# Kernel optimization log

Measured on AMD Instinct MI355X. Metric: run time of the kernel, lower is better.

Reference implementation:

```python
import jax, jax.numpy as jnp
import numpy as np

N_USERS = 50000
N_ENTITIES = 100000
N_RELATIONS = 16
N_KG_EDGES = 2000000
N_UI_EDGES = 1000000
EMB = 64
N_HEADS = 2
D_K = EMB // N_HEADS
N_HOPS = 2


def setup_inputs() -> dict:
    key = jax.random.key(0)
    ks = jax.random.split(key, 8)
    user_emb = jax.random.normal(ks[0], (N_USERS, EMB), dtype=jnp.float32)
    entity_emb = jax.random.normal(ks[1], (N_ENTITIES, EMB), dtype=jnp.float32)
    edge_index = jax.random.randint(ks[2], (2, N_KG_EDGES), 0, N_ENTITIES, dtype=jnp.int64)
    # edge_type values in [1, n_relations] because the module indexes relation_emb[edge_type - 1]
    edge_type = jax.random.randint(ks[3], (N_KG_EDGES,), 1, N_RELATIONS + 1, dtype=jnp.int64)
    inter_user = jax.random.randint(ks[4], (N_UI_EDGES,), 0, N_USERS, dtype=jnp.int64)
    inter_item = jax.random.randint(ks[5], (N_UI_EDGES,), 0, N_ENTITIES, dtype=jnp.int64)
    inter_edge = jnp.stack([inter_user, inter_item], axis=0)
    inter_edge_w = jax.random.uniform(ks[6], (N_UI_EDGES,), dtype=jnp.float32)
    # learned params (xavier-uniform W_Q, normal relation embedding)
    limit = np.sqrt(6.0 / (EMB + EMB)).astype(np.float32)
    W_Q = jax.random.uniform(ks[7], (EMB, EMB), minval=-limit, maxval=limit, dtype=jnp.float32)
    relation_emb = jax.random.normal(jax.random.fold_in(key, 99), (N_RELATIONS, EMB), dtype=jnp.float32)
    return {
        "user_emb": user_emb,
        "entity_emb": entity_emb,
        "edge_index": edge_index,
        "edge_type": edge_type,
        "inter_edge": inter_edge,
        "inter_edge_w": inter_edge_w,
        "W_Q": W_Q,
        "relation_emb": relation_emb,
    }


def _l2norm(x):
    # F.normalize(x) with default p=2, dim=1, eps=1e-12
    n = jnp.sqrt(jnp.sum(x * x, axis=1, keepdims=True))
    return x / jnp.maximum(n, 1e-12)


def reference(user_emb, entity_emb, edge_index, edge_type, inter_edge, inter_edge_w, W_Q, relation_emb):
    n_users = user_emb.shape[0]
    n_entities = entity_emb.shape[0]
    head, tail = edge_index[0], edge_index[1]
    u_idx, i_idx = inter_edge[0], inter_edge[1]
    rel = relation_emb[edge_type - 1]  # [E, d] (constant across hops)
    inv_sqrt_dk = jnp.float32(1.0 / np.sqrt(D_K))

    def hop(u, e):
        # project nodes once, then gather (same math as gather-then-matmul)
        proj = e @ W_Q                                   # [N, d]
        q = proj[head].reshape(-1, N_HEADS, D_K)         # [E, H, dk]
        k = (proj[tail] * rel).reshape(-1, N_HEADS, D_K)
        score = jnp.sum(q * k, axis=-1) * inv_sqrt_dk    # [E, H]
        # scatter_softmax over head segments (max-stabilized)
        smax = jax.ops.segment_max(score, head, num_segments=n_entities)
        ex = jnp.exp(score - smax[head])
        ssum = jax.ops.segment_sum(ex, head, num_segments=n_entities)
        attn = ex / ssum[head]                           # [E, H]
        value = (e[tail] * rel).reshape(-1, N_HEADS, D_K)
        msg = (value * attn[:, :, None]).reshape(-1, EMB)
        e_agg = jax.ops.segment_sum(msg, head, num_segments=n_entities)
        # user aggregation from interaction edges
        item_msg = inter_edge_w[:, None] * e[i_idx]
        u_agg = jax.ops.segment_sum(item_msg, u_idx, num_segments=n_users)
        return e_agg, u_agg

    e_res, u_res = entity_emb, user_emb
    e, u = entity_emb, user_emb
    for _ in range(N_HOPS):
        e, u = hop(u, e)
        # mess_dropout is identity in eval mode
        e = _l2norm(e)
        u = _l2norm(u)
        e_res = e_res + e
        u_res = u_res + u
    return e_res, u_res
```

## Files before the change

### kernel.cpp

```cpp
#include <hip/hip_runtime.h>
#include <math.h>

#define EMB 64
static constexpr float INV_SQRT_DK = 0.17677669529663687f;

#define NBK 128
#define NBU 48
#define P3_PROJ 1024
#define P2PROJ 1024
#define PSHIFT 9
#define PRANGE 512
#define CAPK 14336
#define CAPU 14336

typedef unsigned uint2v __attribute__((ext_vector_type(2)));
typedef float floatx2 __attribute__((ext_vector_type(2)));

__device__ inline unsigned short f2bf(float f) {
    union { float f; unsigned u; } v; v.f = f;
    unsigned r = v.u + 0x7FFF + ((v.u >> 16) & 1);
    return (unsigned short)(r >> 16);
}
__device__ inline float bfhi(unsigned w) {
    union { float f; unsigned u; } v; v.u = w & 0xFFFF0000u; return v.f;
}
__device__ inline float bflo(unsigned w) {
    union { float f; unsigned u; } v; v.u = w << 16; return v.f;
}
__device__ inline float bf2f(unsigned short b) {
    union { float f; unsigned u; } v; v.u = ((unsigned)b) << 16; return v.f;
}
__device__ inline floatx2 fp8lo(unsigned v) {
    return __builtin_amdgcn_cvt_pk_f32_fp8((int)v, false);
}
__device__ inline floatx2 fp8hi(unsigned v) {
    return __builtin_amdgcn_cvt_pk_f32_fp8((int)v, true);
}

template <bool FROM_BF16>
__device__ inline void proj_rows12(const void* __restrict__ ein, const float4* __restrict__ Wl4,
                                   unsigned char* __restrict__ pk12, unsigned* __restrict__ vl,
                                   int n, int g0, int nG, int lane) {
    int rsub = lane >> 4;
    int sub  = lane & 15;
    for (int g = g0; g * 4 < n; g += nG) {
        int r = g * 4 + rsub;
        float x0 = 0.f, x1 = 0.f, x2 = 0.f, x3 = 0.f;
        if (r < n) {
            if (FROM_BF16) {
                ushort4 xv = *(const ushort4*)((const unsigned short*)ein + (size_t)r * EMB + sub * 4);
                x0 = bf2f(xv.x); x1 = bf2f(xv.y); x2 = bf2f(xv.z); x3 = bf2f(xv.w);
            } else {
                float4 xv = *(const float4*)((const float*)ein + (size_t)r * EMB + sub * 4);
                x0 = xv.x; x1 = xv.y; x2 = xv.z; x3 = xv.w;
            }
        }
        float a0 = 0.f, a1 = 0.f, a2 = 0.f, a3 = 0.f;
#pragma unroll
        for (int kb = 0; kb < 16; ++kb) {
            int src = (rsub << 4) | kb;
            float e0 = __shfl(x0, src, 64);
            float e1 = __shfl(x1, src, 64);
            float e2 = __shfl(x2, src, 64);
            float e3 = __shfl(x3, src, 64);
            float4 w0 = Wl4[(kb * 4 + 0) * 16 + sub];
            float4 w1 = Wl4[(kb * 4 + 1) * 16 + sub];
            float4 w2 = Wl4[(kb * 4 + 2) * 16 + sub];
            float4 w3 = Wl4[(kb * 4 + 3) * 16 + sub];
            a0 = fmaf(e0, w0.x, a0); a1 = fmaf(e0, w0.y, a1); a2 = fmaf(e0, w0.z, a2); a3 = fmaf(e0, w0.w, a3);
            a0 = fmaf(e1, w1.x, a0); a1 = fmaf(e1, w1.y, a1); a2 = fmaf(e1, w1.z, a2); a3 = fmaf(e1, w1.w, a3);
            a0 = fmaf(e2, w2.x, a0); a1 = fmaf(e2, w2.y, a1); a2 = fmaf(e2, w2.z, a2); a3 = fmaf(e2, w2.w, a3);
            a0 = fmaf(e3, w3.x, a0); a1 = fmaf(e3, w3.y, a1); a2 = fmaf(e3, w3.z, a2); a3 = fmaf(e3, w3.w, a3);
        }
        if (r < n) {
            unsigned u0 = ((unsigned)f2bf(a1) << 16) | f2bf(a0);
            unsigned u1 = ((unsigned)f2bf(a3) << 16) | f2bf(a2);
            int p8 = __builtin_amdgcn_cvt_pk_fp8_f32(x0, x1, 0, false);
            p8 = __builtin_amdgcn_cvt_pk_fp8_f32(x2, x3, p8, true);
            uint3* dst = (uint3*)(pk12 + (size_t)r * 192 + sub * 12);
            *dst = make_uint3(u0, u1, (unsigned)p8);
            if (vl) vl[(size_t)r * 16 + sub] = (unsigned)p8;
        }
    }
}

__global__ void __launch_bounds__(512) k1_bucket_proj(
        const int* __restrict__ head, const int* __restrict__ tail,
        const int* __restrict__ etype, int E,
        int* __restrict__ pdK, unsigned* __restrict__ bktK,
        const int* __restrict__ iu, const int* __restrict__ ii,
        const float* __restrict__ w, int EI,
        int* __restrict__ pdU, uint2v* __restrict__ bktU,
        const float* __restrict__ e_in, const float* __restrict__ W,
        unsigned char* __restrict__ pk12, unsigned* __restrict__ vl,
        int n_ent, int nPartH, int nPartU) {
    __shared__ float sh[64 * 64];
    int b = blockIdx.x;
    int t = threadIdx.x;
    if (b >= NBK + NBU) {
        for (int i = t; i < 64 * 64; i += 512) sh[i] = W[i];
        __syncthreads();
        int lane = t & 63;
        int g0 = (b - (NBK + NBU)) * 8 + (t >> 6);
        proj_rows12<false>(e_in, (const float4*)sh, pk12, vl, n_ent, g0, P3_PROJ * 8, lane);
        return;
    }
    int* lc = (int*)sh;
    if (t < 256) lc[t] = 0;
    __syncthreads();
    if (b < NBK) {
        int chunk = (E + NBK - 1) / NBK;
        int lo = b * chunk, hi = min(lo + chunk, E);
        for (int e = lo + t; e < hi; e += 512)
            atomicAdd(&lc[__builtin_nontemporal_load(&head[e]) >> PSHIFT], 1);
        __syncthreads();
        if (t < nPartH)
            lc[t] = t * CAPK + atomicAdd(&pdK[t], lc[t]);
        __syncthreads();
        for (int e = lo + t; e < hi; e += 512) {
            int h = __builtin_nontemporal_load(&head[e]);
            int tl = __builtin_nontemporal_load(&tail[e]);
            int ty = __builtin_nontemporal_load(&etype[e]);
            int pos = atomicAdd(&lc[h >> PSHIFT], 1);
            bktK[pos] = ((unsigned)(h & (PRANGE - 1)) << 21) | (unsigned)(tl | ((ty - 1) << 17));
        }
    } else {
        int bb = b - NBK;
        int chunk = (EI + NBU - 1) / NBU;
        int lo = bb * chunk, hi = min(lo + chunk, EI);
        for (int e = lo + t; e < hi; e += 512)
            atomicAdd(&lc[__builtin_nontemporal_load(&iu[e]) >> PSHIFT], 1);
        __syncthreads();
        if (t < nPartU)
            lc[t] = t * CAPU + atomicAdd(&pdU[t], lc[t]);
        __syncthreads();
        for (int e = lo + t; e < hi; e += 512) {
            int u = __builtin_nontemporal_load(&iu[e]);
            int it = __builtin_nontemporal_load(&ii[e]);
            float wv = __builtin_nontemporal_load(&w[e]);
            int pos = atomicAdd(&lc[u >> PSHIFT], 1);
            unsigned wq = (unsigned)(wv * 32767.f + 0.5f);
            uint2v r; r.x = (unsigned)it | (wq << 17); r.y = (unsigned)u;
            bktU[pos] = r;
        }
    }
}

__global__ void __launch_bounds__(512) k2_sort(
        const unsigned* __restrict__ bktK, const int* __restrict__ pdK,
        int* __restrict__ off_h, int* __restrict__ col_h, int n_ent, int nPartH, int E,
        const uint2v* __restrict__ bktU, const int* __restrict__ pdU,
        int* __restrict__ off_u, unsigned* __restrict__ col_ui, int n_usr, int nPartU, int EI) {
    __shared__ int hist[PRANGE];
    __shared__ int wsum[8];
    int t = threadIdx.x;
    int lane = t & 63, wv = t >> 6;
    int b = blockIdx.x;
    bool isU = b >= nPartH;
    int p = isU ? b - nPartH : b;
    const int* pd = isU ? pdU : pdK;
    int cnt = min(pd[p], isU ? CAPU : CAPK);
    int contrib = (t < p) ? pd[t] : 0;
#pragma unroll
    for (int m = 1; m <= 32; m <<= 1) contrib += __shfl_xor(contrib, m, 64);
    if (lane == 0) wsum[wv] = contrib;
    hist[t] = 0;
    __syncthreads();
    int Sp = wsum[0] + wsum[1] + wsum[2] + wsum[3] + wsum[4] + wsum[5] + wsum[6] + wsum[7];
    if (!isU) {
        const unsigned* bk = bktK + (size_t)p * CAPK;
        for (int i = t; i < cnt; i += 512)
            atomicAdd(&hist[__builtin_nontemporal_load(&bk[i]) >> 21], 1);
    } else {
        const uint2v* bu = bktU + (size_t)p * CAPU;
        int plo0 = p << PSHIFT;
        for (int i = t; i < cnt; i += 512) {
            uint2v r = __builtin_nontemporal_load(&bu[i]);
            atomicAdd(&hist[(int)r.y - plo0], 1);
        }
    }
    __syncthreads();
    int v0 = 0, v1 = 0, ps = 0, incl = 0;
    if (t < 256) { v0 = hist[2 * t]; v1 = hist[2 * t + 1]; ps = v0 + v1; incl = ps; }
#pragma unroll
    for (int d = 1; d <= 32; d <<= 1) { int x = __shfl_up(incl, d, 64); if (lane >= d) incl += x; }
    __syncthreads();
    if (t < 256 && lane == 63) wsum[wv] = incl;
    __syncthreads();
    int plo = p << PSHIFT;
    if (t < 256) {
        int woff = 0;
        for (int i = 0; i < wv; ++i) woff += wsum[i];
        int ex = incl - ps + woff;
        int nmax = isU ? n_usr : n_ent;
        int* off = isU ? off_u : off_h;
        if (plo + 2 * t < nmax)     off[plo + 2 * t]     = Sp + ex;
        if (plo + 2 * t + 1 < nmax) off[plo + 2 * t + 1] = Sp + ex + v0;
        hist[2 * t] = Sp + ex;
        hist[2 * t + 1] = Sp + ex + v0;
    }
    if (b == 0 && t == 0) off_h[n_ent] = E;
    if (b == nPartH && t == 0) off_u[n_usr] = EI;
    __syncthreads();
    if (!isU) {
        const unsigned* bk = bktK + (size_t)p * CAPK;
        for (int i = t; i < cnt; i += 512) {
            unsigned r = __builtin_nontemporal_load(&bk[i]);
            int pos = atomicAdd(&hist[r >> 21], 1);
            col_h[pos] = (int)(r & 0x1FFFFFu);
        }
    } else {
        const uint2v* bu = bktU + (size_t)p * CAPU;
        for (int i = t; i < cnt; i += 512) {
            uint2v r = __builtin_nontemporal_load(&bu[i]);
            int pos = atomicAdd(&hist[(int)r.y - plo], 1);
            col_ui[pos] = r.x;
        }
    }
}

#define KG_EDGE12(W, RL, INVD) {                                            \
        float prod = q0 * RL.x * bflo(W.x);                                 \
        prod = fmaf(q1 * RL.y, bfhi(W.x), prod);                            \
        prod = fmaf(q2 * RL.z, bflo(W.y), prod);                            \
        prod = fmaf(q3 * RL.w, bfhi(W.y), prod);                            \
        prod += __shfl_xor(prod, 1, 64);                                    \
        prod += __shfl_xor(prod, 2, 64);                                    \
        prod += __shfl_xor(prod, 4, 64);                                    \
        float ex = __expf(prod * INV_SQRT_DK);                              \
        if (INVD) ex = 0.f;                                                 \
        den += ex;                                                          \
        floatx2 vlo = fp8lo(W.z), vhi = fp8hi(W.z);                         \
        num0 = fmaf(ex * RL.x, vlo.x, num0);                                \
        num1 = fmaf(ex * RL.y, vlo.y, num1);                                \
        num2 = fmaf(ex * RL.z, vhi.x, num2);                                \
        num3 = fmaf(ex * RL.w, vhi.y, num3); }

template <bool HOP1>
__global__ void __launch_bounds__(256) agg_fused_kernel(
        const unsigned char* __restrict__ pk12,
        const unsigned* __restrict__ vl,
        unsigned short* __restrict__ enorm_out,
        const float* __restrict__ rel_emb,
        const int* __restrict__ off_h, const int* __restrict__ col_h,
        const int* __restrict__ off_u, const unsigned* __restrict__ col_ui,
        const float* __restrict__ e_base, float* __restrict__ e_res, int n_ent,
        const float* __restrict__ u_base, float* __restrict__ u_res,
        int n_usr, int kgBlocks, int totalBlocks) {
    __shared__ float4 relS4[16 * 16];
    int bid = blockIdx.x;
    size_t lo = (size_t)bid * kgBlocks / totalBlocks;
    size_t hi = (size_t)(bid + 1) * kgBlocks / totalBlocks;
    int lane = threadIdx.x & 63;
    int wslot = threadIdx.x >> 6;
    int slot = lane >> 4;
    int sub  = lane & 15;
    int dd   = sub * 4;

    if (hi > lo) {
        for (int i = threadIdx.x; i < 16 * 16; i += blockDim.x)
            relS4[i] = ((const float4*)rel_emb)[i];
        __syncthreads();
        int wid = (int)lo * 4 + wslot;
        if (wid >= n_ent) return;
        int s = off_h[wid], e = off_h[wid + 1];
        uint3 qw = *(const uint3*)(pk12 + (size_t)wid * 192 + sub * 12);
        float q0 = bflo(qw.x), q1 = bfhi(qw.x), q2 = bflo(qw.y), q3 = bfhi(qw.y);
        float num0 = 0.f, num1 = 0.f, num2 = 0.f, num3 = 0.f, den = 0.f;
        int j = s;
        for (; j + 15 < e; j += 16) {
            int pA = col_h[j + slot];
            int pB = col_h[j + 4 + slot];
            int pC = col_h[j + 8 + slot];
            int pD = col_h[j + 12 + slot];
            uint3 wA = *(const uint3*)(pk12 + (size_t)(pA & 131071) * 192 + sub * 12);
            uint3 wB = *(const uint3*)(pk12 + (size_t)(pB & 131071) * 192 + sub * 12);
            uint3 wC = *(const uint3*)(pk12 + (size_t)(pC & 131071) * 192 + sub * 12);
            uint3 wD = *(const uint3*)(pk12 + (size_t)(pD & 131071) * 192 + sub * 12);
            float4 rlA = relS4[(pA >> 17) * 16 + sub];
            float4 rlB = relS4[(pB >> 17) * 16 + sub];
            float4 rlC = relS4[(pC >> 17) * 16 + sub];
            float4 rlD = relS4[(pD >> 17) * 16 + sub];
            KG_EDGE12(wA, rlA, false);
            KG_EDGE12(wB, rlB, false);
            KG_EDGE12(wC, rlC, false);
            KG_EDGE12(wD, rlD, false);
        }
        for (; j + 7 < e; j += 8) {
            int pA = col_h[j + slot];
            int pB = col_h[j + 4 + slot];
            uint3 wA = *(const uint3*)(pk12 + (size_t)(pA & 131071) * 192 + sub * 12);
            uint3 wB = *(const uint3*)(pk12 + (size_t)(pB & 131071) * 192 + sub * 12);
            float4 rlA = relS4[(pA >> 17) * 16 + sub];
            float4 rlB = relS4[(pB >> 17) * 16 + sub];
            KG_EDGE12(wA, rlA, false);
            KG_EDGE12(wB, rlB, false);
        }
        for (; j < e; j += 4) {
            int jj = j + slot;
            bool invd = jj >= e;
            if (invd) jj = e - 1;
            int p = col_h[jj];
            uint3 w = *(const uint3*)(pk12 + (size_t)(p & 131071) * 192 + sub * 12);
            float4 rl = relS4[(p >> 17) * 16 + sub];
            KG_EDGE12(w, rl, invd);
        }
        den  += __shfl_xor(den, 16, 64);  den  += __shfl_xor(den, 32, 64);
        num0 += __shfl_xor(num0, 16, 64); num0 += __shfl_xor(num0, 32, 64);
        num1 += __shfl_xor(num1, 16, 64); num1 += __shfl_xor(num1, 32, 64);
        num2 += __shfl_xor(num2, 16, 64); num2 += __shfl_xor(num2, 32, 64);
        num3 += __shfl_xor(num3, 16, 64); num3 += __shfl_xor(num3, 32, 64);
        float dinv = (e > s) ? 1.f / den : 0.f;
        float v0 = num0 * dinv, v1 = num1 * dinv, v2 = num2 * dinv, v3 = num3 * dinv;
        float ss = fmaf(v0, v0, fmaf(v1, v1, fmaf(v2, v2, v3 * v3)));
        ss += __shfl_xor(ss, 1, 64);
        ss += __shfl_xor(ss, 2, 64);
        ss += __shfl_xor(ss, 4, 64);
        ss += __shfl_xor(ss, 8, 64);
        float rn = 1.f / fmaxf(sqrtf(ss), 1e-12f);
        float o0 = v0 * rn, o1 = v1 * rn, o2 = v2 * rn, o3 = v3 * rn;
        if (slot == 0) {
            size_t ix = (size_t)wid * EMB + dd;
            if (HOP1) {
                ushort4 nb; nb.x = f2bf(o0); nb.y = f2bf(o1); nb.z = f2bf(o2); nb.w = f2bf(o3);
                *(ushort4*)&enorm_out[ix] = nb;
                float4 bv = *(const float4*)&e_base[ix];
                *(float4*)&e_res[ix] = make_float4(bv.x + o0, bv.y + o1, bv.z + o2, bv.w + o3);
            } else {
                float4 rv = *(const float4*)&e_res[ix];
                *(float4*)&e_res[ix] = make_float4(rv.x + o0, rv.y + o1, rv.z + o2, rv.w + o3);
            }
        }
    } else if (HOP1) {
        int wid = (bid - (int)lo) * 4 + wslot;
        if (wid >= n_usr) return;
        int s = off_u[wid], e = off_u[wid + 1];
        float a0 = 0.f, a1 = 0.f, a2 = 0.f, a3 = 0.f;
        int j = s;
        for (; j + 7 < e; j += 8) {
            unsigned cA = col_ui[j + slot];
            unsigned cB = col_ui[j + 4 + slot];
            unsigned vA = vl[(size_t)(cA & 131071u) * 16 + sub];
            unsigned vB = vl[(size_t)(cB & 131071u) * 16 + sub];
            float wvA = (cA >> 17) * (1.f / 32767.f);
            float wvB = (cB >> 17) * (1.f / 32767.f);
            floatx2 lA = fp8lo(vA), hA = fp8hi(vA);
            a0 = fmaf(wvA, lA.x, a0); a1 = fmaf(wvA, lA.y, a1);
            a2 = fmaf(wvA, hA.x, a2); a3 = fmaf(wvA, hA.y, a3);
            floatx2 lB = fp8lo(vB), hB = fp8hi(vB);
            a0 = fmaf(wvB, lB.x, a0); a1 = fmaf(wvB, lB.y, a1);
            a2 = fmaf(wvB, hB.x, a2); a3 = fmaf(wvB, hB.y, a3);
        }
        for (; j < e; j += 4) {
            int jj = j + slot;
            bool invd = jj >= e;
            if (invd) jj = e - 1;
            unsigned c = col_ui[jj];
            float wv = invd ? 0.f : (c >> 17) * (1.f / 32767.f);
            unsigned vv = vl[(size_t)(c & 131071u) * 16 + sub];
            floatx2 vlo = fp8lo(vv), vhi = fp8hi(vv);
            a0 = fmaf(wv, vlo.x, a0);
            a1 = fmaf(wv, vlo.y, a1);
            a2 = fmaf(wv, vhi.x, a2);
            a3 = fmaf(wv, vhi.y, a3);
        }
        a0 += __shfl_xor(a0, 16, 64); a0 += __shfl_xor(a0, 32, 64);
        a1 += __shfl_xor(a1, 16, 64); a1 += __shfl_xor(a1, 32, 64);
        a2 += __shfl_xor(a2, 16, 64); a2 += __shfl_xor(a2, 32, 64);
        a3 += __shfl_xor(a3, 16, 64); a3 += __shfl_xor(a3, 32, 64);
        float ss = fmaf(a0, a0, fmaf(a1, a1, fmaf(a2, a2, a3 * a3)));
        ss += __shfl_xor(ss, 1, 64);
        ss += __shfl_xor(ss, 2, 64);
        ss += __shfl_xor(ss, 4, 64);
        ss += __shfl_xor(ss, 8, 64);
        float rn = 1.f / fmaxf(sqrtf(ss), 1e-12f);
        float o0 = a0 * rn, o1 = a1 * rn, o2 = a2 * rn, o3 = a3 * rn;
        if (slot == 0) {
            size_t ix = (size_t)wid * EMB + dd;
            float4 bv = *(const float4*)&u_base[ix];
            *(float4*)&u_res[ix] = make_float4(bv.x + o0, bv.y + o1, bv.z + o2, bv.w + o3);
        }
    }
}

__global__ void __launch_bounds__(256) p2_proj_ui(
        const unsigned short* __restrict__ enorm, const float* __restrict__ W,
        unsigned char* __restrict__ pk12_2, int n_ent,
        const int* __restrict__ off_u, const unsigned* __restrict__ col_ui,
        float* __restrict__ u_res, int n_usr) {
    __shared__ float sh[64 * 64];
    int b = blockIdx.x;
    int lane = threadIdx.x & 63;
    if (b < P2PROJ) {
        for (int i = threadIdx.x; i < 64 * 64; i += 256) sh[i] = W[i];
        __syncthreads();
        int g0 = b * 4 + (threadIdx.x >> 6);
        proj_rows12<true>(enorm, (const float4*)sh, pk12_2, nullptr, n_ent, g0, P2PROJ * 4, lane);
        return;
    }
    int wid = (b - P2PROJ) * 4 + (threadIdx.x >> 6);
    if (wid >= n_usr) return;
    int slot = lane >> 4;
    int sub  = lane & 15;
    int dd   = sub * 4;
    int s = off_u[wid], e = off_u[wid + 1];
    float a0 = 0.f, a1 = 0.f, a2 = 0.f, a3 = 0.f;
    int j = s;
    for (; j + 7 < e; j += 8) {
        unsigned cA = col_ui[j + slot];
        unsigned cB = col_ui[j + 4 + slot];
        ushort4 vA = *(const ushort4*)&enorm[(size_t)(cA & 131071u) * EMB + dd];
        ushort4 vB = *(const ushort4*)&enorm[(size_t)(cB & 131071u) * EMB + dd];
        float wvA = (cA >> 17) * (1.f / 32767.f);
        float wvB = (cB >> 17) * (1.f / 32767.f);
        a0 = fmaf(wvA, bf2f(vA.x), a0); a1 = fmaf(wvA, bf2f(vA.y), a1);
        a2 = fmaf(wvA, bf2f(vA.z), a2); a3 = fmaf(wvA, bf2f(vA.w), a3);
        a0 = fmaf(wvB, bf2f(vB.x), a0); a1 = fmaf(wvB, bf2f(vB.y), a1);
        a2 = fmaf(wvB, bf2f(vB.z), a2); a3 = fmaf(wvB, bf2f(vB.w), a3);
    }
    for (; j < e; j += 4) {
        int jj = j + slot;
        bool invd = jj >= e;
        if (invd) jj = e - 1;
        unsigned c = col_ui[jj];
        float wv = invd ? 0.f : (c >> 17) * (1.f / 32767.f);
        ushort4 v = *(const ushort4*)&enorm[(size_t)(c & 131071u) * EMB + dd];
        a0 = fmaf(wv, bf2f(v.x), a0);
        a1 = fmaf(wv, bf2f(v.y), a1);
        a2 = fmaf(wv, bf2f(v.z), a2);
        a3 = fmaf(wv, bf2f(v.w), a3);
    }
    a0 += __shfl_xor(a0, 16, 64); a0 += __shfl_xor(a0, 32, 64);
    a1 += __shfl_xor(a1, 16, 64); a1 += __shfl_xor(a1, 32, 64);
    a2 += __shfl_xor(a2, 16, 64); a2 += __shfl_xor(a2, 32, 64);
    a3 += __shfl_xor(a3, 16, 64); a3 += __shfl_xor(a3, 32, 64);
    float ss = fmaf(a0, a0, fmaf(a1, a1, fmaf(a2, a2, a3 * a3)));
    ss += __shfl_xor(ss, 1, 64);
    ss += __shfl_xor(ss, 2, 64);
    ss += __shfl_xor(ss, 4, 64);
    ss += __shfl_xor(ss, 8, 64);
    float rn = 1.f / fmaxf(sqrtf(ss), 1e-12f);
    if (slot == 0) {
        size_t ix = (size_t)wid * EMB + dd;
        float4 rv = *(const float4*)&u_res[ix];
        *(float4*)&u_res[ix] = make_float4(rv.x + a0 * rn, rv.y + a1 * rn,
                                           rv.z + a2 * rn, rv.w + a3 * rn);
    }
}

extern "C" void kernel_launch(void* const* d_in, const int* in_sizes, int n_in,
                              void* d_out, int out_size, void* d_ws, size_t ws_size,
                              hipStream_t stream) {
    const float* user_emb   = (const float*)d_in[0];
    const float* entity_emb = (const float*)d_in[1];
    const int*   edge_index = (const int*)d_in[2];
    const int*   edge_type  = (const int*)d_in[3];
    const int*   inter_edge = (const int*)d_in[4];
    const float* inter_w    = (const float*)d_in[5];
    const float* W_Q        = (const float*)d_in[6];
    const float* rel_emb    = (const float*)d_in[7];

    const int E     = in_sizes[3];
    const int EI    = in_sizes[5];
    const int n_ent = in_sizes[1] / EMB;
    const int n_usr = in_sizes[0] / EMB;

    const int* head = edge_index;
    const int* tail = edge_index + E;
    const int* iu   = inter_edge;
    const int* ii   = inter_edge + EI;

    const int nPartH = (n_ent + PRANGE - 1) >> PSHIFT;
    const int nPartU = (n_usr + PRANGE - 1) >> PSHIFT;

    char* ws = (char*)d_ws;
    unsigned char* pk12   = (unsigned char*)ws;  ws += (size_t)n_ent * 192;
    unsigned*      vl     = (unsigned*)ws;       ws += (size_t)n_ent * 64;
    unsigned char* pk12_2 = (unsigned char*)ws;  ws += (size_t)n_ent * 192;
    unsigned short* enorm = (unsigned short*)ws; ws += (size_t)n_ent * EMB * 2;
    int*      col_h  = (int*)ws;               ws += (size_t)E * 4;
    unsigned* col_ui = (unsigned*)ws;          ws += (size_t)EI * 4;
    int*   off_h = (int*)ws;                   ws += (size_t)(n_ent + 1) * 4;
    int*   off_u = (int*)ws;                   ws += (size_t)(n_usr + 1) * 4;
    int*   pdK   = (int*)ws;                   ws += 256 * 4;
    int*   pdU   = (int*)ws;                   ws += 256 * 4;
    unsigned* bktK = (unsigned*)pk12_2;
    uint2v*   bktU = (uint2v*)(bktK + (size_t)nPartH * CAPK);

    float* e_res = (float*)d_out;
    float* u_res = e_res + (size_t)n_ent * EMB;

    hipMemsetAsync(pdK, 0, 512 * 4, stream);
    k1_bucket_proj<<<NBK + NBU + P3_PROJ, 512, 0, stream>>>(
        head, tail, edge_type, E, pdK, bktK,
        iu, ii, inter_w, EI, pdU, bktU,
        entity_emb, W_Q, pk12, vl, n_ent, nPartH, nPartU);
    k2_sort<<<nPartH + nPartU, 512, 0, stream>>>(
        bktK, pdK, off_h, col_h, n_ent, nPartH, E,
        bktU, pdU, off_u, col_ui, n_usr, nPartU, EI);

    const int kgBlocks = (n_ent + 3) / 4;
    const int uiBlocks = (n_usr + 3) / 4;
    const int totalBlocks = kgBlocks + uiBlocks;

    agg_fused_kernel<true><<<totalBlocks, 256, 0, stream>>>(
        pk12, vl, enorm, rel_emb, off_h, col_h, off_u, col_ui,
        entity_emb, e_res, n_ent, user_emb, u_res, n_usr, kgBlocks, totalBlocks);

    p2_proj_ui<<<P2PROJ + uiBlocks, 256, 0, stream>>>(
        enorm, W_Q, pk12_2, n_ent, off_u, col_ui, u_res, n_usr);

    agg_fused_kernel<false><<<kgBlocks, 256, 0, stream>>>(
        pk12_2, nullptr, nullptr, rel_emb, off_h, col_h, nullptr, nullptr,
        nullptr, e_res, n_ent, nullptr, nullptr, 0, kgBlocks, kgBlocks);
}
```

Measured before the change: 404.7 us.

## Move hop-2 user aggregation into second fused kernel using fp8 entity copy

The first aggregation kernel now also writes an fp8-packed copy of the normalized entity embeddings. The hop-2 user aggregation moves out of the projection kernel and into the second fused aggregation kernel, where it reads the compact fp8 values instead of bf16. This leaves the projection kernel lighter and lets the user and KG work share one launch. The cost is an extra fp8 write in hop 1, lower precision for hop-2 user messages, and a dependency on the second kernel's grid balance.

```diff
diff --git a/kernel.cpp b/kernel.cpp
--- a/kernel.cpp
+++ b/kernel.cpp
@@ -241,6 +241,7 @@
         const unsigned char* __restrict__ pk12,
         const unsigned* __restrict__ vl,
         unsigned short* __restrict__ enorm_out,
+        unsigned*       __restrict__ vl2_out,
         const float* __restrict__ rel_emb,
         const int* __restrict__ off_h, const int* __restrict__ col_h,
         const int* __restrict__ off_u, const unsigned* __restrict__ col_ui,
@@ -324,6 +325,9 @@
             if (HOP1) {
                 ushort4 nb; nb.x = f2bf(o0); nb.y = f2bf(o1); nb.z = f2bf(o2); nb.w = f2bf(o3);
                 *(ushort4*)&enorm_out[ix] = nb;
+                int p8 = __builtin_amdgcn_cvt_pk_fp8_f32(o0, o1, 0, false);
+                p8 = __builtin_amdgcn_cvt_pk_fp8_f32(o2, o3, p8, true);
+                vl2_out[(size_t)wid * 16 + sub] = (unsigned)p8;
                 float4 bv = *(const float4*)&e_base[ix];
                 *(float4*)&e_res[ix] = make_float4(bv.x + o0, bv.y + o1, bv.z + o2, bv.w + o3);
             } else {
@@ -331,7 +335,7 @@
                 *(float4*)&e_res[ix] = make_float4(rv.x + o0, rv.y + o1, rv.z + o2, rv.w + o3);
             }
         }
-    } else if (HOP1) {
+    } else {
         int wid = (bid - (int)lo) * 4 + wslot;
         if (wid >= n_usr) return;
         int s = off_u[wid], e = off_u[wid + 1];
@@ -377,75 +381,26 @@
         float o0 = a0 * rn, o1 = a1 * rn, o2 = a2 * rn, o3 = a3 * rn;
         if (slot == 0) {
             size_t ix = (size_t)wid * EMB + dd;
-            float4 bv = *(const float4*)&u_base[ix];
-            *(float4*)&u_res[ix] = make_float4(bv.x + o0, bv.y + o1, bv.z + o2, bv.w + o3);
-        }
-    }
-}
-
-__global__ void __launch_bounds__(256) p2_proj_ui(
+            if (HOP1) {
+                float4 bv = *(const float4*)&u_base[ix];
+                *(float4*)&u_res[ix] = make_float4(bv.x + o0, bv.y + o1, bv.z + o2, bv.w + o3);
+            } else {
+                float4 rv = *(const float4*)&u_res[ix];
+                *(float4*)&u_res[ix] = make_float4(rv.x + o0, rv.y + o1, rv.z + o2, rv.w + o3);
+            }
+        }
+    }
+}
+
+__global__ void __launch_bounds__(256) p2_proj(
         const unsigned short* __restrict__ enorm, const float* __restrict__ W,
-        unsigned char* __restrict__ pk12_2, int n_ent,
-        const int* __restrict__ off_u, const unsigned* __restrict__ col_ui,
-        float* __restrict__ u_res, int n_usr) {
+        unsigned char* __restrict__ pk12_2, int n_ent) {
     __shared__ float sh[64 * 64];
-    int b = blockIdx.x;
+    for (int i = threadIdx.x; i < 64 * 64; i += 256) sh[i] = W[i];
+    __syncthreads();
     int lane = threadIdx.x & 63;
-    if (b < P2PROJ) {
-        for (int i = threadIdx.x; i < 64 * 64; i += 256) sh[i] = W[i];
-        __syncthreads();
-        int g0 = b * 4 + (threadIdx.x >> 6);
-        proj_rows12<true>(enorm, (const float4*)sh, pk12_2, nullptr, n_ent, g0, P2PROJ * 4, lane);
-        return;
-    }
-    int wid = (b - P2PROJ) * 4 + (threadIdx.x >> 6);
-    if (wid >= n_usr) return;
-    int slot = lane >> 4;
-    int sub  = lane & 15;
-    int dd   = sub * 4;
-    int s = off_u[wid], e = off_u[wid + 1];
-    float a0 = 0.f, a1 = 0.f, a2 = 0.f, a3 = 0.f;
-    int j = s;
-    for (; j + 7 < e; j += 8) {
-        unsigned cA = col_ui[j + slot];
-        unsigned cB = col_ui[j + 4 + slot];
-        ushort4 vA = *(const ushort4*)&enorm[(size_t)(cA & 131071u) * EMB + dd];
-        ushort4 vB = *(const ushort4*)&enorm[(size_t)(cB & 131071u) * EMB + dd];
-        float wvA = (cA >> 17) * (1.f / 32767.f);
-        float wvB = (cB >> 17) * (1.f / 32767.f);
-        a0 = fmaf(wvA, bf2f(vA.x), a0); a1 = fmaf(wvA, bf2f(vA.y), a1);
-        a2 = fmaf(wvA, bf2f(vA.z), a2); a3 = fmaf(wvA, bf2f(vA.w), a3);
-        a0 = fmaf(wvB, bf2f(vB.x), a0); a1 = fmaf(wvB, bf2f(vB.y), a1);
-        a2 = fmaf(wvB, bf2f(vB.z), a2); a3 = fmaf(wvB, bf2f(vB.w), a3);
-    }
-    for (; j < e; j += 4) {
-        int jj = j + slot;
-        bool invd = jj >= e;
-        if (invd) jj = e - 1;
-        unsigned c = col_ui[jj];
-        float wv = invd ? 0.f : (c >> 17) * (1.f / 32767.f);
-        ushort4 v = *(const ushort4*)&enorm[(size_t)(c & 131071u) * EMB + dd];
-        a0 = fmaf(wv, bf2f(v.x), a0);
-        a1 = fmaf(wv, bf2f(v.y), a1);
-        a2 = fmaf(wv, bf2f(v.z), a2);
-        a3 = fmaf(wv, bf2f(v.w), a3);
-    }
-    a0 += __shfl_xor(a0, 16, 64); a0 += __shfl_xor(a0, 32, 64);
-    a1 += __shfl_xor(a1, 16, 64); a1 += __shfl_xor(a1, 32, 64);
-    a2 += __shfl_xor(a2, 16, 64); a2 += __shfl_xor(a2, 32, 64);
-    a3 += __shfl_xor(a3, 16, 64); a3 += __shfl_xor(a3, 32, 64);
-    float ss = fmaf(a0, a0, fmaf(a1, a1, fmaf(a2, a2, a3 * a3)));
-    ss += __shfl_xor(ss, 1, 64);
-    ss += __shfl_xor(ss, 2, 64);
-    ss += __shfl_xor(ss, 4, 64);
-    ss += __shfl_xor(ss, 8, 64);
-    float rn = 1.f / fmaxf(sqrtf(ss), 1e-12f);
-    if (slot == 0) {
-        size_t ix = (size_t)wid * EMB + dd;
-        float4 rv = *(const float4*)&u_res[ix];
-        *(float4*)&u_res[ix] = make_float4(rv.x + a0 * rn, rv.y + a1 * rn,
-                                           rv.z + a2 * rn, rv.w + a3 * rn);
-    }
+    int g0 = blockIdx.x * 4 + (threadIdx.x >> 6);
+    proj_rows12<true>(enorm, (const float4*)sh, pk12_2, nullptr, n_ent, g0, P2PROJ * 4, lane);
 }
 
 extern "C" void kernel_launch(void* const* d_in, const int* in_sizes, int n_in,
@@ -476,6 +431,7 @@
     char* ws = (char*)d_ws;
     unsigned char* pk12   = (unsigned char*)ws;  ws += (size_t)n_ent * 192;
     unsigned*      vl     = (unsigned*)ws;       ws += (size_t)n_ent * 64;
+    unsigned*      vl2    = (unsigned*)ws;       ws += (size_t)n_ent * 64;
     unsigned char* pk12_2 = (unsigned char*)ws;  ws += (size_t)n_ent * 192;
     unsigned short* enorm = (unsigned short*)ws; ws += (size_t)n_ent * EMB * 2;
     int*      col_h  = (int*)ws;               ws += (size_t)E * 4;
@@ -504,13 +460,12 @@
     const int totalBlocks = kgBlocks + uiBlocks;
 
     agg_fused_kernel<true><<<totalBlocks, 256, 0, stream>>>(
-        pk12, vl, enorm, rel_emb, off_h, col_h, off_u, col_ui,
+        pk12, vl, enorm, vl2, rel_emb, off_h, col_h, off_u, col_ui,
         entity_emb, e_res, n_ent, user_emb, u_res, n_usr, kgBlocks, totalBlocks);
 
-    p2_proj_ui<<<P2PROJ + uiBlocks, 256, 0, stream>>>(
-        enorm, W_Q, pk12_2, n_ent, off_u, col_ui, u_res, n_usr);
-
-    agg_fused_kernel<false><<<kgBlocks, 256, 0, stream>>>(
-        pk12_2, nullptr, nullptr, rel_emb, off_h, col_h, nullptr, nullptr,
-        nullptr, e_res, n_ent, nullptr, nullptr, 0, kgBlocks, kgBlocks);
-}
+    p2_proj<<<P2PROJ, 256, 0, stream>>>(enorm, W_Q, pk12_2, n_ent);
+
+    agg_fused_kernel<false><<<totalBlocks, 256, 0, stream>>>(
+        pk12_2, vl2, nullptr, nullptr, rel_emb, off_h, col_h, off_u, col_ui,
+        nullptr, e_res, n_ent, nullptr, u_res, n_usr, kgBlocks, totalBlocks);
+}
```

Result: faster. 386.0 us (-4.6%).
